# Performance work log

Measured on AMD Instinct MI355X. Metric: run time of the kernel, lower is better.

## Reference

```python
import jax, jax.numpy as jnp
import numpy as np

B, C, H, W = 8, 128, 128, 128
D_MODEL = C
D_INNER = 2 * D_MODEL          # expand=2 -> 256
D_STATE = 64
HEADDIM = 32                   # _resolve_headdim(128, 32) -> 32
NHEADS = D_INNER // HEADDIM    # 8
D_CONV = 4
CHUNK = 64
GN_GROUPS = 8                  # _group_count(128, 8)
D_XBC = D_INNER + 2 * D_STATE  # 384
D_INPROJ = 2 * D_INNER + 2 * D_STATE + NHEADS  # 648


def _group_norm(x, g, b, groups=GN_GROUPS, eps=1e-5):
    Bn, Cn, Hh, Ww = x.shape
    xr = x.reshape(Bn, groups, Cn // groups, Hh, Ww)
    mu = xr.mean(axis=(2, 3, 4), keepdims=True)
    var = xr.var(axis=(2, 3, 4), keepdims=True)
    xr = (xr - mu) * jax.lax.rsqrt(var + eps)
    return xr.reshape(Bn, Cn, Hh, Ww) * g[None, :, None, None] + b[None, :, None, None]


def _grid_sample_bilinear_border(img, grid):
    # img: (B,C,H,W); grid: (B,H,W,2) with (x,y) in [-1,1]; align_corners=True, border padding
    _, _, Hh, Ww = img.shape
    gx = jnp.clip((grid[..., 0] + 1.0) * 0.5 * (Ww - 1), 0.0, Ww - 1.0)
    gy = jnp.clip((grid[..., 1] + 1.0) * 0.5 * (Hh - 1), 0.0, Hh - 1.0)
    x0 = jnp.floor(gx); y0 = jnp.floor(gy)
    wx = gx - x0; wy = gy - y0
    x0i = x0.astype(jnp.int32); y0i = y0.astype(jnp.int32)
    x1i = jnp.minimum(x0i + 1, Ww - 1); y1i = jnp.minimum(y0i + 1, Hh - 1)
    def per_b(im, y0b, y1b, x0b, x1b, wxb, wyb):
        v00 = im[:, y0b, x0b]; v01 = im[:, y0b, x1b]
        v10 = im[:, y1b, x0b]; v11 = im[:, y1b, x1b]
        return (v00 * (1 - wxb) + v01 * wxb) * (1 - wyb) + (v10 * (1 - wxb) + v11 * wxb) * wyb
    return jax.vmap(per_b)(img, y0i, y1i, x0i, x1i, wx, wy)


def _mamba(seq, in_proj_w, conv_w, conv_b, dt_bias, A_log, D_skip, norm_g, out_w):
    # seq: (Bs, L, d_model) -> (Bs, L, d_model); Mamba2/SSD-style selective scan
    Bs, L, _ = seq.shape
    pad = (CHUNK - L % CHUNK) % CHUNK
    if pad:
        seq = jnp.pad(seq, ((0, 0), (0, pad), (0, 0)))
    Lp = L + pad
    zxbcdt = jnp.einsum('bld,ed->ble', seq, in_proj_w)
    z = zxbcdt[..., :D_INNER]
    xBC = zxbcdt[..., D_INNER:D_INNER + D_XBC]
    dt = jax.nn.softplus(zxbcdt[..., -NHEADS:] + dt_bias)  # (Bs,Lp,nh)
    # causal depthwise conv1d, kernel D_CONV
    xp = jnp.pad(xBC, ((0, 0), (D_CONV - 1, 0), (0, 0)))
    xBC = sum(conv_w[:, k] * xp[:, k:k + Lp, :] for k in range(D_CONV)) + conv_b
    xBC = jax.nn.silu(xBC)
    xs = xBC[..., :D_INNER].reshape(Bs, Lp, NHEADS, HEADDIM)
    Bm = xBC[..., D_INNER:D_INNER + D_STATE]
    Cm = xBC[..., D_INNER + D_STATE:]
    A = -jnp.exp(A_log)  # (nh,)
    def step(h, inp):
        x_t, B_t, C_t, dt_t = inp  # (Bs,nh,hd),(Bs,ds),(Bs,ds),(Bs,nh)
        dA = jnp.exp(dt_t * A)  # (Bs,nh)
        h = h * dA[..., None, None] + (dt_t[..., None] * x_t)[..., None] * B_t[:, None, None, :]
        y = jnp.einsum('bhds,bs->bhd', h, C_t)
        return h, y
    h0 = jnp.zeros((Bs, NHEADS, HEADDIM, D_STATE), seq.dtype)
    _, ys = jax.lax.scan(step, h0, (jnp.moveaxis(xs, 1, 0), jnp.moveaxis(Bm, 1, 0), jnp.moveaxis(Cm, 1, 0), jnp.moveaxis(dt, 1, 0)))
    ys = jnp.moveaxis(ys, 0, 1) + D_skip[None, None, :, None] * xs  # (Bs,Lp,nh,hd)
    y = ys.reshape(Bs, Lp, D_INNER) * jax.nn.silu(z)  # gated
    y = y * jax.lax.rsqrt(jnp.mean(y * y, axis=-1, keepdims=True) + 1e-5) * norm_g  # RMSNorm
    out = jnp.einsum('ble,de->bld', y, out_w)
    return out[:, :L] if pad else out


def _forward(x, dw_w, gn_g, gn_b, pw_w, pw_b, in_proj_w, conv_w, conv_b, dt_bias, A_log, D_skip, norm_g, out_w):
    Bn, Cn, Hh, Ww = x.shape
    dn = ('NCHW', 'OIHW', 'NCHW')
    # offset_net: depthwise 5x5 -> GroupNorm -> GELU -> 1x1
    h1 = jax.lax.conv_general_dilated(x, dw_w, (1, 1), 'SAME', feature_group_count=Cn, dimension_numbers=dn)
    h1 = jax.nn.gelu(_group_norm(h1, gn_g, gn_b), approximate=False)
    off = jax.lax.conv_general_dilated(h1, pw_w, (1, 1), 'SAME', dimension_numbers=dn) + pw_b[None, :, None, None]
    offset = jnp.tanh(off) * min(8.0, max(Hh, Ww) * 0.1)  # (B,1,H,W)
    gy = jnp.linspace(-1.0, 1.0, Hh, dtype=x.dtype)
    gx = jnp.linspace(-1.0, 1.0, Ww, dtype=x.dtype)
    base_y, base_x = jnp.meshgrid(gy, gx, indexing='ij')  # (H,W)
    off_n = offset[:, 0] * (2.0 / max(Hh - 1, 1))  # horizontal scan: vertical offsets
    grid = jnp.stack([jnp.broadcast_to(base_x, (Bn, Hh, Ww)), jnp.clip(base_y + off_n, -1.0, 1.0)], axis=-1)
    deformed = _grid_sample_bilinear_border(x, grid)
    seq = deformed.transpose(0, 2, 3, 1).reshape(Bn * Hh, Ww, Cn)  # (b h) w c
    out = _mamba(seq, in_proj_w, conv_w, conv_b, dt_bias, A_log, D_skip, norm_g, out_w)
    out_2d = out.reshape(Bn, Hh, Ww, Cn).transpose(0, 3, 1, 2)
    return out_2d, offset


def setup_inputs() -> dict:
    key = jax.random.key(0)
    ks = jax.random.split(key, 8)
    return {
        'x': jax.random.normal(ks[0], (B, C, H, W), jnp.float32),
        'dw_w': jax.random.normal(ks[1], (C, 1, 5, 5), jnp.float32) * 0.05,
        'gn_g': jnp.ones((C,), jnp.float32),
        'gn_b': jnp.zeros((C,), jnp.float32),
        'pw_w': jax.random.normal(ks[2], (1, C, 1, 1), jnp.float32) * 0.02,
        'pw_b': jnp.zeros((1,), jnp.float32),
        'in_proj_w': jax.random.normal(ks[3], (D_INPROJ, D_MODEL), jnp.float32) * 0.02,
        'conv_w': jax.random.normal(ks[4], (D_XBC, D_CONV), jnp.float32) * 0.1,
        'conv_b': jnp.zeros((D_XBC,), jnp.float32),
        'dt_bias': jax.random.normal(ks[5], (NHEADS,), jnp.float32) * 0.1,
        'A_log': jnp.log(jnp.arange(1, NHEADS + 1, dtype=jnp.float32)),
        'D_skip': jnp.ones((NHEADS,), jnp.float32),
        'norm_g': jnp.ones((D_INNER,), jnp.float32),
        'out_w': jax.random.normal(ks[6], (D_MODEL, D_INNER), jnp.float32) * 0.02,
    }


def reference(x, dw_w, gn_g, gn_b, pw_w, pw_b, in_proj_w, conv_w, conv_b, dt_bias, A_log, D_skip, norm_g, out_w):
    return _forward(x, dw_w, gn_g, gn_b, pw_w, pw_b, in_proj_w, conv_w, conv_b, dt_bias, A_log, D_skip, norm_g, out_w)
```

## Files before the change

### kernel.cpp

```cpp
#include <hip/hip_runtime.h>
#include <math.h>


typedef _Float16 half8 __attribute__((ext_vector_type(8)));
typedef _Float16 half4 __attribute__((ext_vector_type(4)));
typedef float f32x4 __attribute__((ext_vector_type(4)));

__device__ __forceinline__ float b2f(unsigned short u) {
  return __uint_as_float(((unsigned int)u) << 16);
}
__device__ __forceinline__ bool in_is_f32(const void* gng) {
  return ((const unsigned int*)gng)[0] == 0x3F800000u;
}

#define P_DWW 0
#define P_CW 3200
#define P_CB 4736
#define P_GNG 5120
#define P_GNB 5248
#define P_PWW 5376
#define P_PWB 5504
#define P_DTB 5505
#define P_ALOG 5513
#define P_DSKIP 5521
#define P_NG 5529

__global__ void k_prep_all(const void* dww, const void* cw, const void* cb,
                           const void* gng, const void* gnb, const void* pww,
                           const void* pwb, const void* dtbias, const void* alog,
                           const void* dskip, const void* ng,
                           const void* wproj, const void* outw,
                           float* __restrict__ P, float* __restrict__ gst,
                           _Float16* __restrict__ wprojh, _Float16* __restrict__ outwh) {
  bool f = in_is_f32(gng);
  int stride = gridDim.x * blockDim.x;
  for (int i = blockIdx.x * blockDim.x + threadIdx.x; i < 98304; i += stride) {
    int row = i >> 7;
    float v = 0.f;
    if (row < 648) v = f ? ((const float*)wproj)[i] : b2f(((const unsigned short*)wproj)[i]);
    wprojh[i] = (_Float16)v;
  }
  for (int i = blockIdx.x * blockDim.x + threadIdx.x; i < 32768; i += stride) {
    int e = i & 255;
    float wv = f ? ((const float*)outw)[i] : b2f(((const unsigned short*)outw)[i]);
    float ngv = f ? ((const float*)ng)[e] : b2f(((const unsigned short*)ng)[e]);
    outwh[i] = (_Float16)(wv * ngv);
  }
  if (blockIdx.x == 0) {
    int tid = threadIdx.x;
    if (tid < 128) gst[tid] = 0.f;
    auto cvt = [&](const void* src, int n, int off) {
      for (int i = tid; i < n; i += 256)
        P[off + i] = f ? ((const float*)src)[i] : b2f(((const unsigned short*)src)[i]);
    };
    cvt(dww, 3200, P_DWW);
    cvt(cw, 1536, P_CW);
    cvt(cb, 384, P_CB);
    cvt(gng, 128, P_GNG);
    cvt(gnb, 128, P_GNB);
    cvt(pww, 128, P_PWW);
    cvt(pwb, 1, P_PWB);
    cvt(dtbias, 8, P_DTB);
    cvt(alog, 8, P_ALOG);
    cvt(dskip, 8, P_DSKIP);
    cvt(ng, 256, P_NG);
  }
}

__global__ __launch_bounds__(256) void k_dwconv_v6(const void* __restrict__ x,
                                                   const void* __restrict__ gng,
                                                   const float* __restrict__ P,
                                                   _Float16* __restrict__ h1h,
                                                   float* __restrict__ gst) {
  int bc = blockIdx.x;
  int b = bc >> 7, c = bc & 127;
  bool f32x = in_is_f32(gng);
  __shared__ float red[8];
  const float* xf = (const float*)x + (size_t)bc * 16384;
  const unsigned short* xb = (const unsigned short*)x + (size_t)bc * 16384;
  float w[25];
#pragma unroll
  for (int k = 0; k < 25; ++k) w[k] = P[P_DWW + c * 25 + k];

  int ox = (threadIdx.x & 31) * 4;
  int y0 = (threadIdx.x >> 5) * 16;
  float win[5][12];

  auto loadrow = [&](int gy, float* d) {
#pragma unroll
    for (int k = 0; k < 12; ++k) d[k] = 0.f;
    if (gy >= 0 && gy < 128) {
      if (f32x) {
        const float* rp = xf + gy * 128;
        if (ox >= 4) {
          float4 v = *(const float4*)(rp + ox - 4);
          d[0] = v.x; d[1] = v.y; d[2] = v.z; d[3] = v.w;
        }
        float4 v0 = *(const float4*)(rp + ox);
        d[4] = v0.x; d[5] = v0.y; d[6] = v0.z; d[7] = v0.w;
        if (ox < 124) {
          float4 v1 = *(const float4*)(rp + ox + 4);
          d[8] = v1.x; d[9] = v1.y; d[10] = v1.z; d[11] = v1.w;
        }
      } else {
        const unsigned short* rp = xb + gy * 128;
        if (ox >= 4) {
          ushort4 u = *(const ushort4*)(rp + ox - 4);
          d[0] = b2f(u.x); d[1] = b2f(u.y); d[2] = b2f(u.z); d[3] = b2f(u.w);
        }
        ushort4 u0 = *(const ushort4*)(rp + ox);
        d[4] = b2f(u0.x); d[5] = b2f(u0.y); d[6] = b2f(u0.z); d[7] = b2f(u0.w);
        if (ox < 124) {
          ushort4 u1 = *(const ushort4*)(rp + ox + 4);
          d[8] = b2f(u1.x); d[9] = b2f(u1.y); d[10] = b2f(u1.z); d[11] = b2f(u1.w);
        }
      }
    }
  };

#pragma unroll
  for (int i = 0; i < 4; ++i) loadrow(y0 - 2 + i, win[i]);

  float s = 0.f, sq = 0.f;
  _Float16* hp = h1h + (size_t)bc * 16384;
#pragma unroll
  for (int yo = 0; yo < 16; ++yo) {
    loadrow(y0 + yo + 2, win[(yo + 4) % 5]);
    float o4[4] = {0.f, 0.f, 0.f, 0.f};
#pragma unroll
    for (int ky = 0; ky < 5; ++ky) {
      const float* r = win[(yo + ky) % 5];
#pragma unroll
      for (int j = 0; j < 4; ++j)
#pragma unroll
        for (int kx = 0; kx < 5; ++kx)
          o4[j] += w[ky * 5 + kx] * r[j + kx + 2];
    }
    half4 oh;
#pragma unroll
    for (int j = 0; j < 4; ++j) {
      oh[j] = (_Float16)o4[j];
      s += o4[j]; sq += o4[j] * o4[j];
    }
    *(half4*)&hp[(y0 + yo) * 128 + ox] = oh;
  }

  for (int o = 32; o; o >>= 1) { s += __shfl_down(s, o, 64); sq += __shfl_down(sq, o, 64); }
  int wv = threadIdx.x >> 6;
  if ((threadIdx.x & 63) == 0) { red[wv] = s; red[4 + wv] = sq; }
  __syncthreads();
  if (threadIdx.x == 0) {
    float ts = red[0] + red[1] + red[2] + red[3];
    float tq = red[4] + red[5] + red[6] + red[7];
    int g = (b << 3) + (c >> 4);
    atomicAdd(&gst[g * 2], ts);
    atomicAdd(&gst[g * 2 + 1], tq);
  }
}

__global__ __launch_bounds__(256) void k_gn_part(const _Float16* __restrict__ h1h,
                                                 const float* __restrict__ gst,
                                                 const float* __restrict__ P,
                                                 float* __restrict__ part) {
  int bh2 = blockIdx.x;
  int b = bh2 >> 8;
  int h = (bh2 & 255) >> 1;
  int half = bh2 & 1;
  int tid = threadIdx.x;
  int w = tid & 127;
  int sub = tid >> 7;
  __shared__ float ls[8];
  __shared__ float sacc[2][128];
  if (tid < 4) {
    const float invN = 1.f / 262144.f;
    int g = b * 8 + half * 4 + tid;
    float mean = gst[g * 2] * invN;
    float var = gst[g * 2 + 1] * invN - mean * mean;
    ls[tid * 2] = mean;
    ls[tid * 2 + 1] = rsqrtf(var + 1e-5f);
  }
  __syncthreads();
  int cbase = half * 64 + sub * 32;
  const _Float16* hb = h1h + (((size_t)(b * 128 + cbase)) * 128 + h) * 128 + w;
  float acc = 0.f;
#pragma unroll 4
  for (int ci = 0; ci < 32; ++ci) {
    int c = cbase + ci;
    float v = (float)hb[(size_t)ci * 16384];
    int lg = (sub * 32 + ci) >> 4;
    float nv = (v - ls[lg * 2]) * ls[lg * 2 + 1] * P[P_GNG + c] + P[P_GNB + c];
    float ge = 0.5f * nv * (1.f + erff(nv * 0.70710678118f));
    acc += ge * P[P_PWW + c];
  }
  sacc[sub][w] = acc;
  __syncthreads();
  if (sub == 0) part[(size_t)bh2 * 128 + w] = acc + sacc[1][w];
}

__global__ __launch_bounds__(256) void k_deform_v5(const void* __restrict__ x,
                                                   const void* __restrict__ gng,
                                                   const float* __restrict__ part,
                                                   const float* __restrict__ P,
                                                   _Float16* __restrict__ seqc,
                                                   float* __restrict__ dout,
                                                   int s0) {
  int bh = s0 + blockIdx.x;
  int b = bh >> 7, h = bh & 127;
  int tid = threadIdx.x;
  int w = tid & 127;
  int half = tid >> 7;
  bool f32x = in_is_f32(gng);
  __shared__ float t[128 * 129];
  float ofv = tanhf(part[(size_t)bh * 256 + w] + part[(size_t)bh * 256 + 128 + w] +
                    P[P_PWB]) * 8.0f;
  if (half == 0) dout[16777216 + bh * 128 + w] = ofv;
  float gy = -1.f + (2.f / 127.f) * (float)h + ofv * (2.f / 127.f);
  gy = fminf(fmaxf(gy, -1.f), 1.f);
  float py = (gy + 1.f) * 0.5f * 127.f;
  py = fminf(fmaxf(py, 0.f), 127.f);
  float y0f = floorf(py);
  float wy = py - y0f;
  int y0 = (int)y0f;
  int y1 = min(y0 + 1, 127);
  const float* xfb = (const float*)x + (size_t)b * 128 * 16384;
  const unsigned short* xbb = (const unsigned short*)x + (size_t)b * 128 * 16384;
  int c0 = half * 64;
  for (int i = 0; i < 64; i += 2) {
    int ca = c0 + i, cb2 = c0 + i + 1;
    size_t a0 = (size_t)ca * 16384 + y0 * 128 + w;
    size_t a1 = (size_t)ca * 16384 + y1 * 128 + w;
    size_t b0 = (size_t)cb2 * 16384 + y0 * 128 + w;
    size_t b1 = (size_t)cb2 * 16384 + y1 * 128 + w;
    float va0, va1, vb0, vb1;
    if (f32x) { va0 = xfb[a0]; va1 = xfb[a1]; vb0 = xfb[b0]; vb1 = xfb[b1]; }
    else      { va0 = b2f(xbb[a0]); va1 = b2f(xbb[a1]);
                vb0 = b2f(xbb[b0]); vb1 = b2f(xbb[b1]); }
    t[ca * 129 + w] = va0 + wy * (va1 - va0);
    t[cb2 * 129 + w] = vb0 + wy * (vb1 - vb0);
  }
  __syncthreads();
  int c2 = tid & 127;
  int lb = (tid >> 7) * 64;
  _Float16* sp = seqc + (size_t)blockIdx.x * 16384;
  for (int i = 0; i < 64; ++i) {
    int l = lb + i;
    sp[l * 128 + c2] = (_Float16)t[c2 * 129 + l];
  }
}

__global__ __launch_bounds__(256) void k_gemm1_v7(const _Float16* __restrict__ seqh,
                                                  const _Float16* __restrict__ wprojh,
                                                  const float* __restrict__ P,
                                                  _Float16* __restrict__ zh,
                                                  _Float16* __restrict__ xch,
                                                  float* __restrict__ dtb) {
  __shared__ __align__(16) _Float16 lds[16896];
  _Float16* lA = lds;
  _Float16* lB = lds + 8192;
  int m0 = blockIdx.x * 128;
  int e0 = blockIdx.y * 128;
  int tid = threadIdx.x;
  int lane = tid & 63;
  int wv = tid >> 6;
  f32x4 acc[2][8];
#pragma unroll
  for (int rf = 0; rf < 2; ++rf)
#pragma unroll
    for (int cf = 0; cf < 8; ++cf) acc[rf][cf] = (f32x4){0.f, 0.f, 0.f, 0.f};

  int rsel = lane & 15, q = lane >> 4;
  for (int k0 = 0; k0 < 128; k0 += 64) {
    if (k0) __syncthreads();
#pragma unroll
    for (int p = 0; p < 4; ++p) {
      int idx = tid + 256 * p;
      int row = idx >> 3, ch = idx & 7;
      int dch = ch ^ (row & 7);
      *(half8*)&lA[row * 64 + dch * 8] =
          *(const half8*)&seqh[(size_t)(m0 + row) * 128 + k0 + ch * 8];
      *(half8*)&lB[row * 64 + dch * 8] =
          *(const half8*)&wprojh[(size_t)(e0 + row) * 128 + k0 + ch * 8];
    }
    __syncthreads();
#pragma unroll
    for (int kk = 0; kk < 2; ++kk) {
      half8 a[2];
#pragma unroll
      for (int rf = 0; rf < 2; ++rf) {
        int row = wv * 32 + rf * 16 + rsel;
        int ch = (kk * 4 + q) ^ (row & 7);
        a[rf] = *(const half8*)&lA[row * 64 + ch * 8];
      }
#pragma unroll
      for (int cf = 0; cf < 8; ++cf) {
        int row = cf * 16 + rsel;
        int ch = (kk * 4 + q) ^ (row & 7);
        half8 b = *(const half8*)&lB[row * 64 + ch * 8];
        acc[0][cf] = __builtin_amdgcn_mfma_f32_16x16x32_f16(a[0], b, acc[0][cf], 0, 0, 0);
        acc[1][cf] = __builtin_amdgcn_mfma_f32_16x16x32_f16(a[1], b, acc[1][cf], 0, 0, 0);
      }
    }
  }

  if (e0 < 256) {
#pragma unroll
    for (int rf = 0; rf < 2; ++rf) {
      int mb = m0 + wv * 32 + rf * 16 + q * 4;
#pragma unroll
      for (int cf = 0; cf < 8; ++cf) {
        _Float16* pz = zh + (size_t)mb * 256 + e0 + cf * 16 + rsel;
#pragma unroll
        for (int r = 0; r < 4; ++r) pz[(size_t)r * 256] = (_Float16)acc[rf][cf][r];
      }
    }
  } else if (e0 < 640) {
    __syncthreads();
#pragma unroll
    for (int rf = 0; rf < 2; ++rf) {
#pragma unroll
      for (int r = 0; r < 4; ++r) {
        int row = wv * 32 + rf * 16 + q * 4 + r;
#pragma unroll
        for (int cf = 0; cf < 8; ++cf)
          lds[row * 132 + cf * 16 + rsel] = (_Float16)acc[rf][cf][r];
      }
    }
    __syncthreads();
    int cc = tid & 127;
    int rh = tid >> 7;
    int eg = (e0 - 256) + cc;
    float w0 = P[P_CW + eg * 4 + 0], w1 = P[P_CW + eg * 4 + 1];
    float w2 = P[P_CW + eg * 4 + 2], w3 = P[P_CW + eg * 4 + 3];
    float bb = P[P_CB + eg];
    int r0 = rh * 64;
    float x0 = (r0 >= 3) ? (float)lds[(r0 - 3) * 132 + cc] : 0.f;
    float x1 = (r0 >= 2) ? (float)lds[(r0 - 2) * 132 + cc] : 0.f;
    float x2 = (r0 >= 1) ? (float)lds[(r0 - 1) * 132 + cc] : 0.f;
    _Float16* xo = xch + (size_t)m0 * 384 + eg;
    for (int r = r0; r < r0 + 64; ++r) {
      float x3 = (float)lds[r * 132 + cc];
      float a = bb + w0 * x0 + w1 * x1 + w2 * x2 + w3 * x3;
      xo[(size_t)r * 384] = (_Float16)(a / (1.f + __expf(-a)));
      x0 = x1; x1 = x2; x2 = x3;
    }
  } else {
#pragma unroll
    for (int rf = 0; rf < 2; ++rf) {
      int mb = m0 + wv * 32 + rf * 16 + q * 4;
      if (rsel < 8) {
        float bias = P[P_DTB + rsel];
#pragma unroll
        for (int r = 0; r < 4; ++r) {
          float dv = acc[rf][0][r] + bias;
          float sp = (dv > 20.f) ? dv : log1pf(__expf(dv));
          dtb[(size_t)(mb + r) * 8 + rsel] = sp;
        }
      }
    }
  }
}

__global__ __launch_bounds__(256) void k_ssd_v4(const _Float16* __restrict__ xch,
                                                const _Float16* __restrict__ zh,
                                                const float* __restrict__ dtb,
                                                const float* __restrict__ P,
                                                _Float16* __restrict__ ys,
                                                float* __restrict__ rr) {
  int seq = blockIdx.x;
  int tid = threadIdx.x;
  int lane = tid & 63, wv = tid >> 6;
  int rsel = lane & 15, q = lane >> 4;
  __shared__ __align__(16) _Float16 G[128 * 128];
  __shared__ __align__(16) _Float16 Xt[32 * 128];
  __shared__ float dts[128 * 8];
  __shared__ float Ts[8 * 128];
  __shared__ float ejs[128];
  const _Float16* xb = xch + (size_t)seq * 49152;
  const _Float16* zb = zh + (size_t)seq * 32768;
  const float* dtp = dtb + (size_t)seq * 1024;

  for (int i = tid; i < 1024; i += 256) dts[i] = dtp[i];
  __syncthreads();
  if (tid < 8) {
    float a = 0.f;
    for (int l = 0; l < 128; ++l) { a += dts[l * 8 + tid]; Ts[tid * 128 + l] = a; }
  }

  f32x4 gacc[2][8];
#pragma unroll
  for (int rf = 0; rf < 2; ++rf)
#pragma unroll
    for (int cf = 0; cf < 8; ++cf) gacc[rf][cf] = (f32x4){0.f, 0.f, 0.f, 0.f};
#pragma unroll
  for (int kk = 0; kk < 2; ++kk) {
    half8 a[2];
#pragma unroll
    for (int rf = 0; rf < 2; ++rf) {
      int l = wv * 32 + rf * 16 + rsel;
      a[rf] = *(const half8*)&xb[(size_t)l * 384 + 320 + kk * 32 + q * 8];
    }
#pragma unroll
    for (int cf = 0; cf < 8; ++cf) {
      int j = cf * 16 + rsel;
      half8 b = *(const half8*)&xb[(size_t)j * 384 + 256 + kk * 32 + q * 8];
      gacc[0][cf] = __builtin_amdgcn_mfma_f32_16x16x32_f16(a[0], b, gacc[0][cf], 0, 0, 0);
      gacc[1][cf] = __builtin_amdgcn_mfma_f32_16x16x32_f16(a[1], b, gacc[1][cf], 0, 0, 0);
    }
  }
#pragma unroll
  for (int rf = 0; rf < 2; ++rf) {
#pragma unroll
    for (int r = 0; r < 4; ++r) {
      int l = wv * 32 + rf * 16 + q * 4 + r;
#pragma unroll
      for (int cf = 0; cf < 8; ++cf) {
        int j = cf * 16 + rsel;
        G[l * 128 + (((j >> 3) ^ (l & 7)) << 3) + (j & 7)] = (_Float16)gacc[rf][cf][r];
      }
    }
  }
  __syncthreads();

  float ssq[2][4];
#pragma unroll
  for (int rf = 0; rf < 2; ++rf)
#pragma unroll
    for (int r = 0; r < 4; ++r) ssq[rf][r] = 0.f;

  _Float16* yp = ys + (size_t)seq * 32768;
  for (int h = 0; h < 8; ++h) {
    float Ah = -__expf(P[P_ALOG + h]);
    float Dk = P[P_DSKIP + h];
    {
      int j = tid >> 1, ds = (tid & 1) * 16;
      float dtj = dts[j * 8 + h];
      half8 v0 = *(const half8*)&xb[(size_t)j * 384 + h * 32 + ds];
      half8 v1 = *(const half8*)&xb[(size_t)j * 384 + h * 32 + ds + 8];
#pragma unroll
      for (int e = 0; e < 8; ++e) {
        int d0 = ds + e, d1 = ds + 8 + e;
        Xt[d0 * 128 + (((j >> 3) ^ (d0 & 7)) << 3) + (j & 7)] = (_Float16)((float)v0[e] * dtj);
        Xt[d1 * 128 + (((j >> 3) ^ (d1 & 7)) << 3) + (j & 7)] = (_Float16)((float)v1[e] * dtj);
      }
      if (tid < 128) {
        float TE = Ts[h * 128 + ((tid >> 5) << 5) + 31];
        ejs[tid] = __expf(Ah * (TE - Ts[h * 128 + tid]));
      }
    }
    __syncthreads();
    f32x4 acc[2][2];
#pragma unroll
    for (int rf = 0; rf < 2; ++rf)
#pragma unroll
      for (int cf = 0; cf < 2; ++cf) acc[rf][cf] = (f32x4){0.f, 0.f, 0.f, 0.f};
#pragma unroll
    for (int kk = 0; kk < 4; ++kk) {
      if (kk <= wv) {
        int jb = kk * 32 + q * 8;
        int chk = kk * 4 + q;
        half8 a[2];
        if (kk == wv) {
          float4 tj0 = *(const float4*)&Ts[h * 128 + jb];
          float4 tj1 = *(const float4*)&Ts[h * 128 + jb + 4];
          float tj[8] = {tj0.x, tj0.y, tj0.z, tj0.w, tj1.x, tj1.y, tj1.z, tj1.w};
#pragma unroll
          for (int rf = 0; rf < 2; ++rf) {
            int l = wv * 32 + rf * 16 + rsel;
            half8 g = *(const half8*)&G[l * 128 + ((chk ^ (l & 7)) << 3)];
            float Tl = Ts[h * 128 + l];
            half8 w;
#pragma unroll
            for (int e = 0; e < 8; ++e) {
              int j = jb + e;
              float m = (j <= l) ? __expf(Ah * (Tl - tj[e])) : 0.f;
              w[e] = (_Float16)((float)g[e] * m);
            }
            a[rf] = w;
          }
        } else {
          float TE = Ts[h * 128 + kk * 32 + 31];
          float4 e0v = *(const float4*)&ejs[jb];
          float4 e1v = *(const float4*)&ejs[jb + 4];
          float ej[8] = {e0v.x, e0v.y, e0v.z, e0v.w, e1v.x, e1v.y, e1v.z, e1v.w};
#pragma unroll
          for (int rf = 0; rf < 2; ++rf) {
            int l = wv * 32 + rf * 16 + rsel;
            half8 g = *(const half8*)&G[l * 128 + ((chk ^ (l & 7)) << 3)];
            float el = __expf(Ah * (Ts[h * 128 + l] - TE));
            half8 w;
#pragma unroll
            for (int e = 0; e < 8; ++e)
              w[e] = (_Float16)((float)g[e] * el * ej[e]);
            a[rf] = w;
          }
        }
#pragma unroll
        for (int cf = 0; cf < 2; ++cf) {
          int d = cf * 16 + rsel;
          half8 b = *(const half8*)&Xt[d * 128 + ((chk ^ (d & 7)) << 3)];
          acc[0][cf] = __builtin_amdgcn_mfma_f32_16x16x32_f16(a[0], b, acc[0][cf], 0, 0, 0);
          acc[1][cf] = __builtin_amdgcn_mfma_f32_16x16x32_f16(a[1], b, acc[1][cf], 0, 0, 0);
        }
      }
    }
#pragma unroll
    for (int rf = 0; rf < 2; ++rf) {
      int lb = wv * 32 + rf * 16 + q * 4;
#pragma unroll
      for (int cf = 0; cf < 2; ++cf) {
        int d = cf * 16 + rsel;
#pragma unroll
        for (int r = 0; r < 4; ++r) {
          int l = lb + r;
          float xv = (float)xb[(size_t)l * 384 + h * 32 + d];
          float zv = (float)zb[(size_t)l * 256 + h * 32 + d];
          float y = acc[rf][cf][r] + Dk * xv;
          float yg = y * (zv / (1.f + __expf(-zv)));
          ssq[rf][r] += yg * yg;
          yp[(size_t)l * 256 + h * 32 + d] = (_Float16)yg;
        }
      }
    }
    __syncthreads();
  }

  float* rp = rr + (size_t)seq * 128;
#pragma unroll
  for (int rf = 0; rf < 2; ++rf) {
#pragma unroll
    for (int r = 0; r < 4; ++r) {
      float ss = ssq[rf][r];
      ss += __shfl_xor(ss, 1, 64);
      ss += __shfl_xor(ss, 2, 64);
      ss += __shfl_xor(ss, 4, 64);
      ss += __shfl_xor(ss, 8, 64);
      if (rsel == 0) rp[wv * 32 + rf * 16 + q * 4 + r] = rsqrtf(ss * (1.f / 256.f) + 1e-5f);
    }
  }
}

__global__ __launch_bounds__(256) void k_gemm2_v4(const _Float16* __restrict__ ysg,
                                                  const float* __restrict__ rr,
                                                  const _Float16* __restrict__ outwh,
                                                  float* __restrict__ dout,
                                                  int tok0) {
  __shared__ __align__(16) _Float16 lA[128 * 64];
  __shared__ __align__(16) _Float16 lB[64 * 64];
  int t0 = blockIdx.x * 64;
  int tid = threadIdx.x;
  int lane = tid & 63;
  int wv = tid >> 6;
  f32x4 acc[2][4];
#pragma unroll
  for (int rf = 0; rf < 2; ++rf)
#pragma unroll
    for (int cf = 0; cf < 4; ++cf) acc[rf][cf] = (f32x4){0.f, 0.f, 0.f, 0.f};

  int rsel = lane & 15, q = lane >> 4;
  for (int k0 = 0; k0 < 256; k0 += 64) {
    if (k0) __syncthreads();
#pragma unroll
    for (int p = 0; p < 4; ++p) {
      int idx = tid + 256 * p;
      int row = idx >> 3, ch = idx & 7;
      int dch = ch ^ (row & 7);
      *(half8*)&lA[row * 64 + dch * 8] =
          *(const half8*)&outwh[(size_t)row * 256 + k0 + ch * 8];
    }
#pragma unroll
    for (int p = 0; p < 2; ++p) {
      int idx = tid + 256 * p;
      int row = idx >> 3, ch = idx & 7;
      int dch = ch ^ (row & 7);
      float rv = rr[t0 + row];
      half8 v = *(const half8*)&ysg[(size_t)(t0 + row) * 256 + k0 + ch * 8];
      half8 o;
#pragma unroll
      for (int e = 0; e < 8; ++e) o[e] = (_Float16)((float)v[e] * rv);
      *(half8*)&lB[row * 64 + dch * 8] = o;
    }
    __syncthreads();
#pragma unroll
    for (int kk = 0; kk < 2; ++kk) {
      half8 a[2];
#pragma unroll
      for (int rf = 0; rf < 2; ++rf) {
        int row = wv * 32 + rf * 16 + rsel;
        int ch = (kk * 4 + q) ^ (row & 7);
        a[rf] = *(const half8*)&lA[row * 64 + ch * 8];
      }
#pragma unroll
      for (int cf = 0; cf < 4; ++cf) {
        int row = cf * 16 + rsel;
        int ch = (kk * 4 + q) ^ (row & 7);
        half8 b = *(const half8*)&lB[row * 64 + ch * 8];
        acc[0][cf] = __builtin_amdgcn_mfma_f32_16x16x32_f16(a[0], b, acc[0][cf], 0, 0, 0);
        acc[1][cf] = __builtin_amdgcn_mfma_f32_16x16x32_f16(a[1], b, acc[1][cf], 0, 0, 0);
      }
    }
  }

  int l0 = tok0 + t0;
  int b = l0 >> 14;
  int rem0 = l0 & 16383;
#pragma unroll
  for (int rf = 0; rf < 2; ++rf) {
    int cbase = wv * 32 + rf * 16 + q * 4;
#pragma unroll
    for (int cf = 0; cf < 4; ++cf) {
#pragma unroll
      for (int r = 0; r < 4; ++r) {
        dout[(size_t)(b * 128 + cbase + r) * 16384 + rem0 + cf * 16 + rsel] = acc[rf][cf][r];
      }
    }
  }
}

extern "C" void kernel_launch(void* const* d_in, const int* in_sizes, int n_in,
                              void* d_out, int out_size, void* d_ws, size_t ws_size,
                              hipStream_t stream) {
  const void* x      = d_in[0];
  const void* dww    = d_in[1];
  const void* gng    = d_in[2];
  const void* gnb    = d_in[3];
  const void* pww    = d_in[4];
  const void* pwb    = d_in[5];
  const void* wproj  = d_in[6];
  const void* cw     = d_in[7];
  const void* cb     = d_in[8];
  const void* dtbias = d_in[9];
  const void* alog   = d_in[10];
  const void* dskip  = d_in[11];
  const void* ng     = d_in[12];
  const void* outw   = d_in[13];
  float* out = (float*)d_out;

  char* ws = (char*)d_ws;
  float* gst        = (float*)(ws + 0);
  float* P          = (float*)(ws + 8192);
  _Float16* wprojh  = (_Float16*)(ws + 40960);
  _Float16* outwh   = (_Float16*)(ws + 372736);
  float* part       = (float*)(ws + 503808);
  char* cbase       = ws + 1552384;

  _Float16* h1h = (_Float16*)out;

  const int opts[11] = {1024, 512, 256, 128, 64, 32, 16, 8, 4, 2, 1};
  int CH = 1;
  for (int i = 0; i < 11; ++i) {
    if (1552384ull + (unsigned long long)opts[i] * 266752ull <= (unsigned long long)ws_size) {
      CH = opts[i];
      break;
    }
  }
  int NC = 1024 / CH;

  _Float16* seqh = (_Float16*)(cbase);
  _Float16* zh   = (_Float16*)(cbase + (size_t)CH * 32768);
  _Float16* xch  = (_Float16*)(cbase + (size_t)CH * 98304);
  float* dtbf    = (float*)(cbase + (size_t)CH * 196608);
  _Float16* ysh  = (_Float16*)(cbase + (size_t)CH * 200704);
  float* rrf     = (float*)(cbase + (size_t)CH * 266240);

  k_prep_all<<<128, 256, 0, stream>>>(dww, cw, cb, gng, gnb, pww, pwb, dtbias,
                                      alog, dskip, ng, wproj, outw, P, gst,
                                      wprojh, outwh);
  k_dwconv_v6<<<1024, 256, 0, stream>>>(x, gng, P, h1h, gst);
  k_gn_part<<<2048, 256, 0, stream>>>(h1h, gst, P, part);

  int M = CH * 128;
  for (int c = 0; c < NC; ++c) {
    int s0 = c * CH;
    k_deform_v5<<<CH, 256, 0, stream>>>(x, gng, part, P, seqh, out, s0);
    k_gemm1_v7<<<dim3(M / 128, 6), 256, 0, stream>>>(seqh, wprojh, P, zh, xch, dtbf);
    k_ssd_v4<<<CH, 256, 0, stream>>>(xch, zh, dtbf, P, ysh, rrf);
    k_gemm2_v4<<<dim3(M / 64), 256, 0, stream>>>(ysh, rrf, outwh, out, s0 * 128);
  }
}
```

Before: 468.5 us.

## Widen in_proj GEMM blocks to 256 columns sharing one A tile

The in_proj GEMM now runs 512-thread blocks that each cover 256 output columns. Two 256-thread groups share one staged activation tile, which halves the grid and the repeated A loads from global memory. In the block that holds the dt columns, the dt group skips the MFMAs for unused column fragments. The SiLU division becomes a hardware reciprocal. The larger LDS footprint (about 66 KB per block) and bigger blocks may lower occupancy, and the dt block's two groups now do uneven amounts of work.

```diff
diff --git a/kernel.cpp b/kernel.cpp
--- a/kernel.cpp
+++ b/kernel.cpp
@@ -248,36 +248,47 @@
   }
 }
 
-__global__ __launch_bounds__(256) void k_gemm1_v7(const _Float16* __restrict__ seqh,
+__global__ __launch_bounds__(512) void k_gemm1_v8(const _Float16* __restrict__ seqh,
                                                   const _Float16* __restrict__ wprojh,
                                                   const float* __restrict__ P,
                                                   _Float16* __restrict__ zh,
                                                   _Float16* __restrict__ xch,
                                                   float* __restrict__ dtb) {
-  __shared__ __align__(16) _Float16 lds[16896];
+  __shared__ __align__(16) _Float16 lds[33792];
   _Float16* lA = lds;
   _Float16* lB = lds + 8192;
   int m0 = blockIdx.x * 128;
-  int e0 = blockIdx.y * 128;
+  int e0 = blockIdx.y * 256;
   int tid = threadIdx.x;
   int lane = tid & 63;
   int wv = tid >> 6;
+  int grp = tid >> 8;
+  int wvl = wv & 3;
+  int rsel = lane & 15, q = lane >> 4;
+  bool isz = (e0 == 0);
+  bool isdt = (e0 == 512) && (grp == 1);
+
   f32x4 acc[2][8];
 #pragma unroll
   for (int rf = 0; rf < 2; ++rf)
 #pragma unroll
     for (int cf = 0; cf < 8; ++cf) acc[rf][cf] = (f32x4){0.f, 0.f, 0.f, 0.f};
 
-  int rsel = lane & 15, q = lane >> 4;
   for (int k0 = 0; k0 < 128; k0 += 64) {
     if (k0) __syncthreads();
 #pragma unroll
-    for (int p = 0; p < 4; ++p) {
-      int idx = tid + 256 * p;
+    for (int p = 0; p < 2; ++p) {
+      int idx = tid + 512 * p;
       int row = idx >> 3, ch = idx & 7;
       int dch = ch ^ (row & 7);
       *(half8*)&lA[row * 64 + dch * 8] =
           *(const half8*)&seqh[(size_t)(m0 + row) * 128 + k0 + ch * 8];
+    }
+#pragma unroll
+    for (int p = 0; p < 4; ++p) {
+      int idx = tid + 512 * p;
+      int row = idx >> 3, ch = idx & 7;
+      int dch = ch ^ (row & 7);
       *(half8*)&lB[row * 64 + dch * 8] =
           *(const half8*)&wprojh[(size_t)(e0 + row) * 128 + k0 + ch * 8];
     }
@@ -287,13 +298,14 @@
       half8 a[2];
 #pragma unroll
       for (int rf = 0; rf < 2; ++rf) {
-        int row = wv * 32 + rf * 16 + rsel;
+        int row = wvl * 32 + rf * 16 + rsel;
         int ch = (kk * 4 + q) ^ (row & 7);
         a[rf] = *(const half8*)&lA[row * 64 + ch * 8];
       }
 #pragma unroll
       for (int cf = 0; cf < 8; ++cf) {
-        int row = cf * 16 + rsel;
+        if (isdt && cf > 0) continue;
+        int row = grp * 128 + cf * 16 + rsel;
         int ch = (kk * 4 + q) ^ (row & 7);
         half8 b = *(const half8*)&lB[row * 64 + ch * 8];
         acc[0][cf] = __builtin_amdgcn_mfma_f32_16x16x32_f16(a[0], b, acc[0][cf], 0, 0, 0);
@@ -302,60 +314,65 @@
     }
   }
 
-  if (e0 < 256) {
+  __syncthreads();
+  _Float16* sx = lds + grp * 16896;
+  if (!isz && !isdt) {
 #pragma unroll
     for (int rf = 0; rf < 2; ++rf) {
-      int mb = m0 + wv * 32 + rf * 16 + q * 4;
+#pragma unroll
+      for (int r = 0; r < 4; ++r) {
+        int row = wvl * 32 + rf * 16 + q * 4 + r;
+#pragma unroll
+        for (int cf = 0; cf < 8; ++cf)
+          sx[row * 132 + cf * 16 + rsel] = (_Float16)acc[rf][cf][r];
+      }
+    }
+  }
+  __syncthreads();
+
+  if (isz) {
+#pragma unroll
+    for (int rf = 0; rf < 2; ++rf) {
+      int mb = m0 + wvl * 32 + rf * 16 + q * 4;
 #pragma unroll
       for (int cf = 0; cf < 8; ++cf) {
-        _Float16* pz = zh + (size_t)mb * 256 + e0 + cf * 16 + rsel;
+        _Float16* pz = zh + (size_t)mb * 256 + grp * 128 + cf * 16 + rsel;
 #pragma unroll
         for (int r = 0; r < 4; ++r) pz[(size_t)r * 256] = (_Float16)acc[rf][cf][r];
       }
     }
-  } else if (e0 < 640) {
-    __syncthreads();
+  } else if (isdt) {
 #pragma unroll
     for (int rf = 0; rf < 2; ++rf) {
-#pragma unroll
-      for (int r = 0; r < 4; ++r) {
-        int row = wv * 32 + rf * 16 + q * 4 + r;
-#pragma unroll
-        for (int cf = 0; cf < 8; ++cf)
-          lds[row * 132 + cf * 16 + rsel] = (_Float16)acc[rf][cf][r];
-      }
-    }
-    __syncthreads();
-    int cc = tid & 127;
-    int rh = tid >> 7;
-    int eg = (e0 - 256) + cc;
+      int mb = m0 + wvl * 32 + rf * 16 + q * 4;
+      if (rsel < 8) {
+        float bias = P[P_DTB + rsel];
+#pragma unroll
+        for (int r = 0; r < 4; ++r) {
+          float dv = acc[rf][0][r] + bias;
+          float sp = (dv > 20.f) ? dv : log1pf(__expf(dv));
+          dtb[(size_t)(mb + r) * 8 + rsel] = sp;
+        }
+      }
+    }
+  } else {
+    int tg = tid & 255;
+    int cc = tg & 127;
+    int rh = tg >> 7;
+    int eg = (e0 - 256) + grp * 128 + cc;
     float w0 = P[P_CW + eg * 4 + 0], w1 = P[P_CW + eg * 4 + 1];
     float w2 = P[P_CW + eg * 4 + 2], w3 = P[P_CW + eg * 4 + 3];
     float bb = P[P_CB + eg];
     int r0 = rh * 64;
-    float x0 = (r0 >= 3) ? (float)lds[(r0 - 3) * 132 + cc] : 0.f;
-    float x1 = (r0 >= 2) ? (float)lds[(r0 - 2) * 132 + cc] : 0.f;
-    float x2 = (r0 >= 1) ? (float)lds[(r0 - 1) * 132 + cc] : 0.f;
+    float x0 = (r0 >= 3) ? (float)sx[(r0 - 3) * 132 + cc] : 0.f;
+    float x1 = (r0 >= 2) ? (float)sx[(r0 - 2) * 132 + cc] : 0.f;
+    float x2 = (r0 >= 1) ? (float)sx[(r0 - 1) * 132 + cc] : 0.f;
     _Float16* xo = xch + (size_t)m0 * 384 + eg;
     for (int r = r0; r < r0 + 64; ++r) {
-      float x3 = (float)lds[r * 132 + cc];
+      float x3 = (float)sx[r * 132 + cc];
       float a = bb + w0 * x0 + w1 * x1 + w2 * x2 + w3 * x3;
-      xo[(size_t)r * 384] = (_Float16)(a / (1.f + __expf(-a)));
+      xo[(size_t)r * 384] = (_Float16)(a * __builtin_amdgcn_rcpf(1.f + __expf(-a)));
       x0 = x1; x1 = x2; x2 = x3;
-    }
-  } else {
-#pragma unroll
-    for (int rf = 0; rf < 2; ++rf) {
-      int mb = m0 + wv * 32 + rf * 16 + q * 4;
-      if (rsel < 8) {
-        float bias = P[P_DTB + rsel];
-#pragma unroll
-        for (int r = 0; r < 4; ++r) {
-          float dv = acc[rf][0][r] + bias;
-          float sp = (dv > 20.f) ? dv : log1pf(__expf(dv));
-          dtb[(size_t)(mb + r) * 8 + rsel] = sp;
-        }
-      }
     }
   }
 }
@@ -672,7 +689,7 @@
   for (int c = 0; c < NC; ++c) {
     int s0 = c * CH;
     k_deform_v5<<<CH, 256, 0, stream>>>(x, gng, part, P, seqh, out, s0);
-    k_gemm1_v7<<<dim3(M / 128, 6), 256, 0, stream>>>(seqh, wprojh, P, zh, xch, dtbf);
+    k_gemm1_v8<<<dim3(M / 128, 3), 512, 0, stream>>>(seqh, wprojh, P, zh, xch, dtbf);
     k_ssd_v4<<<CH, 256, 0, stream>>>(xch, zh, dtbf, P, ysh, rrf);
     k_gemm2_v4<<<dim3(M / 64), 256, 0, stream>>>(ysh, rrf, outwh, out, s0 * 128);
   }
```

Result: faster. 449.3 us (median of 3 runs) (-4.1%).
